# Performance work log

Hardware: AMD Instinct MI355X
Metric: run time of the kernel (lower is better)

The kernel has to match this reference:

```python
import jax, jax.numpy as jnp
import numpy as np

B, H, S, D = 2, 16, 2048, 64


def setup_inputs() -> dict:
    key = jax.random.key(0)
    kq, kk, kv = jax.random.split(key, 3)
    Q = jax.random.normal(kq, (B, H, S, D), dtype=jnp.float32)
    K = jax.random.normal(kk, (B, H, S, D), dtype=jnp.float32)
    V = jax.random.normal(kv, (B, H, S, D), dtype=jnp.float32)
    # causal mask: True = masked out (matches torch masked_fill_ semantics)
    causal = ~jnp.tril(jnp.ones((S, S), dtype=bool))
    mask = jnp.broadcast_to(causal, (B, H, S, S))
    return {"Q": Q, "K": K, "V": V, "mask": mask}


def reference(Q, K, V, mask):
    d_q = Q.shape[-1]
    scale = 1.0 / np.sqrt(d_q).astype(np.float32)
    # scores: (B, H, S, S)
    scores = jnp.einsum('bhqd,bhkd->bhqk', Q, K) * scale
    scores = jnp.where(mask, jnp.float32(-1e9), scores)
    attention = jax.nn.softmax(scores, axis=-1)
    context = jnp.einsum('bhqk,bhkd->bhqd', attention, V)
    return (context, attention)
```

## Files before the change

kernel.cpp:

```cpp
#include <hip/hip_runtime.h>
#include <hip/hip_bf16.h>


constexpr int SEQ = 2048;
constexpr int HD  = 64;
constexpr int NHEADS = 32;
constexpr int QT  = 64;
constexpr int NT  = SEQ / QT;

typedef __bf16 bf16x8 __attribute__((ext_vector_type(8)));
typedef unsigned short u16x8 __attribute__((ext_vector_type(8)));
typedef unsigned short u16x4 __attribute__((ext_vector_type(4)));
typedef float f32x4 __attribute__((ext_vector_type(4)));
typedef unsigned short us;

__device__ __forceinline__ us f2bf(float x) {
  unsigned u = __builtin_bit_cast(unsigned, x);
  return (us)((u + 0x7fffu + ((u >> 16) & 1u)) >> 16);
}
__device__ __forceinline__ float bf2f(us b) {
  return __builtin_bit_cast(float, (unsigned)b << 16);
}

#define GLOAD_LDS(gp, lp)                                                        \
  __builtin_amdgcn_global_load_lds(                                             \
      (const __attribute__((address_space(1))) void*)(gp),                      \
      (__attribute__((address_space(3))) void*)(lp), 16, 0, 0)

__device__ __forceinline__ void stage8k(const us* img, us* lds, int w, int l) {
  const char* g = (const char*)img + w * 2048 + l * 16;
  char* s = (char*)lds + w * 2048;
  GLOAD_LDS(g, s);
  GLOAD_LDS(g + 1024, s + 1024);
}

__global__ void prep_kernel(const float* __restrict__ Qg,
                            const float* __restrict__ Kg,
                            const float* __restrict__ Vg,
                            us* __restrict__ ws) {
  const int tile = blockIdx.x & (NT - 1);
  const int bh   = blockIdx.x >> 5;
  const int t = threadIdx.x;
  const size_t tOff = ((size_t)bh * SEQ + (size_t)tile * QT) * HD;
  us* Qi = ws + ((size_t)bh * NT + tile) * 4096;
  us* Ki = Qi + (size_t)NHEADS * NT * 4096;
  us* Vi = Ki + (size_t)NHEADS * NT * 4096;

  #pragma unroll
  for (int g0 = 0; g0 < 2; ++g0) {
    const int g = t + 256 * g0;
    const int r = g >> 3, c8 = g & 7;
    const int cp = (8 * c8) ^ ((r & 7) << 3);
    const float* qs = Qg + tOff + (size_t)r * HD + cp;
    const float* ks = Kg + tOff + (size_t)r * HD + cp;
    u16x8 q, k;
    #pragma unroll
    for (int j = 0; j < 8; ++j) { q[j] = f2bf(qs[j]); k[j] = f2bf(ks[j]); }
    *(u16x8*)(Qi + 8 * g) = q;
    *(u16x8*)(Ki + 8 * g) = k;
  }
  #pragma unroll
  for (int g0 = 0; g0 < 2; ++g0) {
    const int g = t + 256 * g0;
    const int d = g >> 3, k8 = g & 7;
    const int kp = (8 * k8) ^ ((d & 7) << 3);
    const float* vs = Vg + tOff + d;
    u16x8 v;
    #pragma unroll
    for (int j = 0; j < 8; ++j) v[j] = f2bf(vs[(size_t)(kp + j) * HD]);
    *(u16x8*)(Vi + 8 * g) = v;
  }
}

__launch_bounds__(256, 3)
__global__ void attn_main(const us* __restrict__ ws, float* __restrict__ out) {
  const int fb = blockIdx.x;
  const int bh = fb & (NHEADS - 1);
  const int pi = fb >> 5;
  const int t  = threadIdx.x;
  const int l  = t & 63;
  const int w  = t >> 6;
  const int l16 = l & 15;
  const int lg  = l >> 4;

  __shared__ __align__(16) us Ks[2][4096];
  __shared__ __align__(16) us Vs[2][4096];
  __shared__ __align__(16) us Ps[4][1024];

  const us* Qi = ws + (size_t)bh * NT * 4096;
  const us* Ki = Qi + (size_t)NHEADS * NT * 4096;
  const us* Vi = Ki + (size_t)NHEADS * NT * 4096;

  float* ctx = out + (size_t)bh * SEQ * HD;
  float* att = out + (size_t)NHEADS * SEQ * HD + (size_t)bh * SEQ * SEQ;

  const float KC = 0.18033688011112042f;

  for (int half = 0; half < 2; ++half) {
    const int qt = half ? (NT - 1 - pi) : pi;
    const int qbase = qt * QT;
    const int qg = qbase + w * 16 + l16;

    stage8k(Ki, Ks[0], w, l);
    bf16x8 aq[2];
    {
      const int qr = w * 16 + l16;
      #pragma unroll
      for (int ks = 0; ks < 2; ++ks) {
        const int idx = (qr * 64 + ks * 32 + lg * 8) ^ ((qr & 7) << 3);
        aq[ks] = __builtin_bit_cast(bf16x8, *(const u16x8*)(&Qi[(size_t)qt * 4096 + idx]));
      }
    }
    {
      const int zc0 = (qt + 1) * QT;
      const int nz4 = (SEQ - zc0) >> 2;
      for (int rr = 0; rr < QT; ++rr) {
        float* rowp = att + (size_t)(qbase + rr) * SEQ + zc0;
        for (int c = t; c < nz4; c += 256)
          __builtin_nontemporal_store((f32x4){0.f, 0.f, 0.f, 0.f}, (f32x4*)(rowp + 4 * c));
      }
    }
    __syncthreads();

    float rsum = 0.f;
    {
      int cur = 0;
      for (int kt = 0; kt <= qt; ++kt) {
        if (kt < qt) stage8k(Ki + (size_t)(kt + 1) * 4096, Ks[cur ^ 1], w, l);
        const us* krb = Ks[cur];
        const int kb = kt * QT;
        #pragma unroll
        for (int ct = 0; ct < 4; ++ct) {
          f32x4 acc = {0.f, 0.f, 0.f, 0.f};
          #pragma unroll
          for (int ks = 0; ks < 2; ++ks) {
            const int kr = ct * 16 + l16;
            const int idx = (kr * 64 + ks * 32 + lg * 8) ^ ((kr & 7) << 3);
            bf16x8 bk = __builtin_bit_cast(bf16x8, *(const u16x8*)(&krb[idx]));
            acc = __builtin_amdgcn_mfma_f32_16x16x32_bf16(bk, aq[ks], acc, 0, 0, 0);
          }
          const int kg0 = kb + ct * 16 + lg * 4;
          #pragma unroll
          for (int rr = 0; rr < 4; ++rr) {
            float e = __builtin_amdgcn_exp2f(acc[rr] * KC);
            rsum += (kg0 + rr <= qg) ? e : 0.f;
          }
        }
        __syncthreads();
        cur ^= 1;
      }
    }
    stage8k(Ki, Ks[0], w, l);
    stage8k(Vi, Vs[0], w, l);
    rsum += __shfl_xor(rsum, 16);
    rsum += __shfl_xor(rsum, 32);
    const float inv = 1.f / rsum;
    __syncthreads();

    f32x4 oacc[4];
    #pragma unroll
    for (int ct = 0; ct < 4; ++ct) oacc[ct] = (f32x4){0.f, 0.f, 0.f, 0.f};

    {
      int cur = 0;
      for (int kt = 0; kt <= qt; ++kt) {
        if (kt < qt) {
          stage8k(Ki + (size_t)(kt + 1) * 4096, Ks[cur ^ 1], w, l);
          stage8k(Vi + (size_t)(kt + 1) * 4096, Vs[cur ^ 1], w, l);
        }
        __builtin_amdgcn_sched_barrier(0);
        const us* krb = Ks[cur];
        const us* vrb = Vs[cur];
        const int kb = kt * QT;

        #pragma unroll
        for (int ct = 0; ct < 4; ++ct) {
          f32x4 acc = {0.f, 0.f, 0.f, 0.f};
          #pragma unroll
          for (int ks = 0; ks < 2; ++ks) {
            const int kr = ct * 16 + l16;
            const int idx = (kr * 64 + ks * 32 + lg * 8) ^ ((kr & 7) << 3);
            bf16x8 bk = __builtin_bit_cast(bf16x8, *(const u16x8*)(&krb[idx]));
            acc = __builtin_amdgcn_mfma_f32_16x16x32_bf16(bk, aq[ks], acc, 0, 0, 0);
          }
          const int kg0 = kb + ct * 16 + lg * 4;
          u16x4 pb;
          #pragma unroll
          for (int rr = 0; rr < 4; ++rr) {
            float e = __builtin_amdgcn_exp2f(acc[rr] * KC) * inv;
            pb[rr] = f2bf((kg0 + rr <= qg) ? e : 0.f);
          }
          const int pidx = (l16 * 64 + ct * 16 + lg * 4) ^ ((l16 & 7) << 3);
          *(u16x4*)(&Ps[w][pidx]) = pb;
        }

        #pragma unroll
        for (int j = 0; j < 4; ++j) {
          const int rloc = lg + 4 * j;
          const int idx = (rloc * 64 + 4 * l16) ^ ((rloc & 7) << 3);
          u16x4 p4 = *(const u16x4*)(&Ps[w][idx]);
          f32x4 pv = { bf2f(p4[0]), bf2f(p4[1]), bf2f(p4[2]), bf2f(p4[3]) };
          __builtin_nontemporal_store(pv,
              (f32x4*)(att + (size_t)(qbase + w * 16 + rloc) * SEQ + kb + 4 * l16));
        }

        bf16x8 pa[2];
        #pragma unroll
        for (int ks = 0; ks < 2; ++ks) {
          const int pidx = (l16 * 64 + ks * 32 + lg * 8) ^ ((l16 & 7) << 3);
          pa[ks] = __builtin_bit_cast(bf16x8, *(const u16x8*)(&Ps[w][pidx]));
        }
        #pragma unroll
        for (int ct = 0; ct < 4; ++ct) {
          #pragma unroll
          for (int ks = 0; ks < 2; ++ks) {
            const int dr = ct * 16 + l16;
            const int vidx = (dr * 64 + ks * 32 + lg * 8) ^ ((dr & 7) << 3);
            bf16x8 av = __builtin_bit_cast(bf16x8, *(const u16x8*)(&vrb[vidx]));
            oacc[ct] = __builtin_amdgcn_mfma_f32_16x16x32_bf16(av, pa[ks], oacc[ct], 0, 0, 0);
          }
        }

        if (kt < qt) {
          asm volatile("s_waitcnt vmcnt(4) lgkmcnt(0)" ::: "memory");
        } else {
          asm volatile("s_waitcnt lgkmcnt(0)" ::: "memory");
        }
        __builtin_amdgcn_s_barrier();
        __builtin_amdgcn_sched_barrier(0);
        cur ^= 1;
      }
    }

    #pragma unroll
    for (int ct = 0; ct < 4; ++ct)
      __builtin_nontemporal_store(oacc[ct],
          (f32x4*)(ctx + (size_t)qg * HD + ct * 16 + lg * 4));
  }
}

__launch_bounds__(256, 2)
__global__ void attn_fallback(const float* __restrict__ Qg,
                              const float* __restrict__ Kg,
                              const float* __restrict__ Vg,
                              float* __restrict__ out) {
  const int fb = blockIdx.x;
  const int bh = fb & (NHEADS - 1);
  const int pi = fb >> 5;
  const int t  = threadIdx.x;
  const int l  = t & 63;
  const int w  = t >> 6;
  const int l16 = l & 15;
  const int lg  = l >> 4;

  __shared__ __align__(16) us Qs[QT * HD];
  __shared__ __align__(16) us Ks[QT * HD];
  __shared__ __align__(16) us Vs[QT * HD];
  __shared__ __align__(16) us Ps[4][16 * QT];

  const size_t hoff = (size_t)bh * SEQ * HD;
  const float* Qh = Qg + hoff;
  const float* Kh = Kg + hoff;
  const float* Vh = Vg + hoff;
  float* ctx = out + hoff;
  float* att = out + (size_t)NHEADS * SEQ * HD + (size_t)bh * SEQ * SEQ;

  auto load_tile = [&](const float* src, f32x4 (&reg)[4]) {
    #pragma unroll
    for (int j = 0; j < 4; ++j) {
      const int f = t + 256 * j;
      reg[j] = *(const f32x4*)(src + (size_t)(f >> 4) * HD + 4 * (f & 15));
    }
  };
  auto write_k = [&](const f32x4 (&reg)[4], us* dst) {
    #pragma unroll
    for (int j = 0; j < 4; ++j) {
      const int f = t + 256 * j;
      const int rr = f >> 4, c4 = f & 15;
      const int idx = (rr * 64 + 4 * c4) ^ ((rr & 7) << 3);
      u16x4 b = { f2bf(reg[j].x), f2bf(reg[j].y), f2bf(reg[j].z), f2bf(reg[j].w) };
      *(u16x4*)(&dst[idx]) = b;
    }
  };
  auto write_vv = [&](const f32x4 (&reg)[4], us* dst) {
    #pragma unroll
    for (int j = 0; j < 4; ++j) {
      const int f = t + 256 * j;
      const int rr = f >> 4, c4 = f & 15;
      const int idx = (rr * 64 + 4 * c4) ^ (((rr >> 3) & 3) << 4);
      u16x4 b = { f2bf(reg[j].x), f2bf(reg[j].y), f2bf(reg[j].z), f2bf(reg[j].w) };
      *(u16x4*)(&dst[idx]) = b;
    }
  };

  const float sc = 0.125f;

  for (int half = 0; half < 2; ++half) {
    const int qt = half ? (NT - 1 - pi) : pi;
    const int qbase = qt * QT;
    const int qg = qbase + w * 16 + l16;

    __syncthreads();
    {
      const int zc0 = (qt + 1) * QT;
      const int nz4 = (SEQ - zc0) >> 2;
      for (int rr = 0; rr < QT; ++rr) {
        float* rowp = att + (size_t)(qbase + rr) * SEQ + zc0;
        for (int c = t; c < nz4; c += 256)
          __builtin_nontemporal_store((f32x4){0.f, 0.f, 0.f, 0.f}, (f32x4*)(rowp + 4 * c));
      }
    }
    {
      f32x4 qreg[4];
      load_tile(Qh + (size_t)qbase * HD, qreg);
      write_k(qreg, Qs);
    }
    __syncthreads();

    bf16x8 aq[2];
    #pragma unroll
    for (int ks = 0; ks < 2; ++ks) {
      const int qr = w * 16 + l16;
      const int idx = (qr * 64 + ks * 32 + lg * 8) ^ ((qr & 7) << 3);
      aq[ks] = __builtin_bit_cast(bf16x8, *(const u16x8*)(&Qs[idx]));
    }

    float rsum = 0.f;
    {
      f32x4 kreg[4];
      load_tile(Kh, kreg);
      write_k(kreg, Ks);
      __syncthreads();
      for (int kt = 0; kt <= qt; ++kt) {
        if (kt < qt) load_tile(Kh + (size_t)(kt + 1) * QT * HD, kreg);
        const int kb = kt * QT;
        #pragma unroll
        for (int ct = 0; ct < 4; ++ct) {
          f32x4 acc = {0.f, 0.f, 0.f, 0.f};
          #pragma unroll
          for (int ks = 0; ks < 2; ++ks) {
            const int kr = ct * 16 + l16;
            const int idx = (kr * 64 + ks * 32 + lg * 8) ^ ((kr & 7) << 3);
            bf16x8 bk = __builtin_bit_cast(bf16x8, *(const u16x8*)(&Ks[idx]));
            acc = __builtin_amdgcn_mfma_f32_16x16x32_bf16(bk, aq[ks], acc, 0, 0, 0);
          }
          const int kg0 = kb + ct * 16 + lg * 4;
          #pragma unroll
          for (int rr = 0; rr < 4; ++rr) {
            float e = __expf(acc[rr] * sc);
            rsum += (kg0 + rr <= qg) ? e : 0.f;
          }
        }
        __syncthreads();
        if (kt < qt) write_k(kreg, Ks);
        __syncthreads();
      }
    }
    rsum += __shfl_xor(rsum, 16);
    rsum += __shfl_xor(rsum, 32);
    const float inv = 1.f / rsum;

    f32x4 oacc[4];
    #pragma unroll
    for (int ct = 0; ct < 4; ++ct) oacc[ct] = (f32x4){0.f, 0.f, 0.f, 0.f};

    {
      f32x4 kreg[4], vreg[4];
      load_tile(Kh, kreg);
      load_tile(Vh, vreg);
      write_k(kreg, Ks);
      write_vv(vreg, Vs);
      __syncthreads();
      for (int kt = 0; kt <= qt; ++kt) {
        if (kt < qt) {
          load_tile(Kh + (size_t)(kt + 1) * QT * HD, kreg);
          load_tile(Vh + (size_t)(kt + 1) * QT * HD, vreg);
        }
        const int kb = kt * QT;
        #pragma unroll
        for (int ct = 0; ct < 4; ++ct) {
          f32x4 acc = {0.f, 0.f, 0.f, 0.f};
          #pragma unroll
          for (int ks = 0; ks < 2; ++ks) {
            const int kr = ct * 16 + l16;
            const int idx = (kr * 64 + ks * 32 + lg * 8) ^ ((kr & 7) << 3);
            bf16x8 bk = __builtin_bit_cast(bf16x8, *(const u16x8*)(&Ks[idx]));
            acc = __builtin_amdgcn_mfma_f32_16x16x32_bf16(bk, aq[ks], acc, 0, 0, 0);
          }
          const int kg0 = kb + ct * 16 + lg * 4;
          u16x4 pb;
          #pragma unroll
          for (int rr = 0; rr < 4; ++rr) {
            float e = __expf(acc[rr] * sc) * inv;
            pb[rr] = f2bf((kg0 + rr <= qg) ? e : 0.f);
          }
          const int pidx = (l16 * 64 + ct * 16 + lg * 4) ^ ((l16 & 7) << 3);
          *(u16x4*)(&Ps[w][pidx]) = pb;
        }
        #pragma unroll
        for (int ct = 0; ct < 4; ++ct) {
          #pragma unroll
          for (int ks = 0; ks < 2; ++ks) {
            const int key0 = ks * 32 + lg * 8;
            const int pidx = (l16 * 64 + key0) ^ ((l16 & 7) << 3);
            bf16x8 pa = __builtin_bit_cast(bf16x8, *(const u16x8*)(&Ps[w][pidx]));
            bf16x8 av;
            const int dcol = ct * 16 + l16;
            const int xorv = ((key0 >> 3) & 3) << 4;
            #pragma unroll
            for (int j = 0; j < 8; ++j)
              av[j] = __builtin_bit_cast(__bf16, Vs[((key0 + j) * 64 + dcol) ^ xorv]);
            oacc[ct] = __builtin_amdgcn_mfma_f32_16x16x32_bf16(av, pa, oacc[ct], 0, 0, 0);
          }
        }
        __syncthreads();
        #pragma unroll
        for (int j = 0; j < 4; ++j) {
          const int f = t + 256 * j;
          const int rr = f >> 4, c4 = f & 15;
          const int ww = rr >> 4, qr = rr & 15;
          const int idx = (qr * 64 + 4 * c4) ^ ((qr & 7) << 3);
          u16x4 pb = *(const u16x4*)(&Ps[ww][idx]);
          f32x4 pv = { bf2f(pb[0]), bf2f(pb[1]), bf2f(pb[2]), bf2f(pb[3]) };
          __builtin_nontemporal_store(pv,
              (f32x4*)(att + (size_t)(qbase + rr) * SEQ + kb + 4 * c4));
        }
        if (kt < qt) {
          write_k(kreg, Ks);
          write_vv(vreg, Vs);
        }
        __syncthreads();
      }
    }
    #pragma unroll
    for (int ct = 0; ct < 4; ++ct)
      *(f32x4*)(ctx + (size_t)qg * HD + ct * 16 + lg * 4) = oacc[ct];
  }
}

extern "C" void kernel_launch(void* const* d_in, const int* in_sizes, int n_in,
                              void* d_out, int out_size, void* d_ws, size_t ws_size,
                              hipStream_t stream) {
  const float* Q = (const float*)d_in[0];
  const float* K = (const float*)d_in[1];
  const float* V = (const float*)d_in[2];
  float* out = (float*)d_out;
  const size_t NEED = (size_t)3 * NHEADS * NT * 4096 * sizeof(us);
  if (ws_size >= NEED && d_ws != nullptr) {
    us* wsp = (us*)d_ws;
    prep_kernel<<<dim3(NHEADS * NT), dim3(256), 0, stream>>>(Q, K, V, wsp);
    attn_main<<<dim3(NT / 2 * NHEADS), dim3(256), 0, stream>>>(wsp, out);
  } else {
    attn_fallback<<<dim3(NT / 2 * NHEADS), dim3(256), 0, stream>>>(Q, K, V, out);
  }
}
```

Measured before the change: 145.4 us.

## Fuse row-sum passes for paired low/high query tiles and remap block order

Each block now handles its low and high causal query tiles together. It computes both tiles' softmax denominators in one sweep over K, so the low tile reuses the K tiles staged for the high tile instead of loading them again. Block-to-tile mapping is also permuted so that the upper half of the grid walks tiles in reverse order. The manual waitcnt/s_barrier pipelining in the P·V phase is replaced by a plain __syncthreads, which may lose overlap. Holding two sets of Q fragments and accumulators raises register pressure.

```diff
diff --git a/kernel.cpp b/kernel.cpp
--- a/kernel.cpp
+++ b/kernel.cpp
@@ -76,7 +76,9 @@
 __global__ void attn_main(const us* __restrict__ ws, float* __restrict__ out) {
   const int fb = blockIdx.x;
   const int bh = fb & (NHEADS - 1);
-  const int pi = fb >> 5;
+  const int pr = (fb >> 5) & 7;
+  const int pi = (fb >> 8) ? (15 - pr) : pr;
+  const int lo = pi, hi = NT - 1 - pi;
   const int t  = threadIdx.x;
   const int l  = t & 63;
   const int w  = t >> 6;
@@ -96,147 +98,163 @@
 
   const float KC = 0.18033688011112042f;
 
-  for (int half = 0; half < 2; ++half) {
-    const int qt = half ? (NT - 1 - pi) : pi;
-    const int qbase = qt * QT;
-    const int qg = qbase + w * 16 + l16;
-
-    stage8k(Ki, Ks[0], w, l);
-    bf16x8 aq[2];
-    {
-      const int qr = w * 16 + l16;
-      #pragma unroll
-      for (int ks = 0; ks < 2; ++ks) {
-        const int idx = (qr * 64 + ks * 32 + lg * 8) ^ ((qr & 7) << 3);
-        aq[ks] = __builtin_bit_cast(bf16x8, *(const u16x8*)(&Qi[(size_t)qt * 4096 + idx]));
-      }
-    }
-    {
+  bf16x8 aql[2], aqh[2];
+  {
+    const int qr = w * 16 + l16;
+    #pragma unroll
+    for (int ks = 0; ks < 2; ++ks) {
+      const int idx = (qr * 64 + ks * 32 + lg * 8) ^ ((qr & 7) << 3);
+      aql[ks] = __builtin_bit_cast(bf16x8, *(const u16x8*)(&Qi[(size_t)lo * 4096 + idx]));
+      aqh[ks] = __builtin_bit_cast(bf16x8, *(const u16x8*)(&Qi[(size_t)hi * 4096 + idx]));
+    }
+  }
+  const int qg_lo = lo * QT + w * 16 + l16;
+  const int qg_hi = hi * QT + w * 16 + l16;
+
+  stage8k(Ki, Ks[0], w, l);
+  {
+    auto zfill = [&](int qt) {
+      const int qb = qt * QT;
       const int zc0 = (qt + 1) * QT;
       const int nz4 = (SEQ - zc0) >> 2;
       for (int rr = 0; rr < QT; ++rr) {
-        float* rowp = att + (size_t)(qbase + rr) * SEQ + zc0;
+        float* rowp = att + (size_t)(qb + rr) * SEQ + zc0;
         for (int c = t; c < nz4; c += 256)
           __builtin_nontemporal_store((f32x4){0.f, 0.f, 0.f, 0.f}, (f32x4*)(rowp + 4 * c));
       }
-    }
-    __syncthreads();
-
-    float rsum = 0.f;
-    {
-      int cur = 0;
-      for (int kt = 0; kt <= qt; ++kt) {
-        if (kt < qt) stage8k(Ki + (size_t)(kt + 1) * 4096, Ks[cur ^ 1], w, l);
-        const us* krb = Ks[cur];
-        const int kb = kt * QT;
-        #pragma unroll
-        for (int ct = 0; ct < 4; ++ct) {
-          f32x4 acc = {0.f, 0.f, 0.f, 0.f};
-          #pragma unroll
-          for (int ks = 0; ks < 2; ++ks) {
-            const int kr = ct * 16 + l16;
-            const int idx = (kr * 64 + ks * 32 + lg * 8) ^ ((kr & 7) << 3);
-            bf16x8 bk = __builtin_bit_cast(bf16x8, *(const u16x8*)(&krb[idx]));
-            acc = __builtin_amdgcn_mfma_f32_16x16x32_bf16(bk, aq[ks], acc, 0, 0, 0);
-          }
-          const int kg0 = kb + ct * 16 + lg * 4;
-          #pragma unroll
-          for (int rr = 0; rr < 4; ++rr) {
-            float e = __builtin_amdgcn_exp2f(acc[rr] * KC);
-            rsum += (kg0 + rr <= qg) ? e : 0.f;
-          }
-        }
-        __syncthreads();
-        cur ^= 1;
-      }
-    }
-    stage8k(Ki, Ks[0], w, l);
-    stage8k(Vi, Vs[0], w, l);
-    rsum += __shfl_xor(rsum, 16);
-    rsum += __shfl_xor(rsum, 32);
-    const float inv = 1.f / rsum;
-    __syncthreads();
-
+    };
+    zfill(lo);
+    zfill(hi);
+  }
+  __syncthreads();
+
+  float rs_lo = 0.f, rs_hi = 0.f;
+  {
+    int cur = 0;
+    for (int kt = 0; kt <= hi; ++kt) {
+      if (kt < hi) stage8k(Ki + (size_t)(kt + 1) * 4096, Ks[cur ^ 1], w, l);
+      const us* krb = Ks[cur];
+      const int kb = kt * QT;
+      const bool loact = (kt <= lo);
+      #pragma unroll
+      for (int ct = 0; ct < 4; ++ct) {
+        f32x4 acch = {0.f, 0.f, 0.f, 0.f};
+        f32x4 accl = {0.f, 0.f, 0.f, 0.f};
+        #pragma unroll
+        for (int ks = 0; ks < 2; ++ks) {
+          const int kr = ct * 16 + l16;
+          const int idx = (kr * 64 + ks * 32 + lg * 8) ^ ((kr & 7) << 3);
+          bf16x8 bk = __builtin_bit_cast(bf16x8, *(const u16x8*)(&krb[idx]));
+          acch = __builtin_amdgcn_mfma_f32_16x16x32_bf16(bk, aqh[ks], acch, 0, 0, 0);
+          if (loact)
+            accl = __builtin_amdgcn_mfma_f32_16x16x32_bf16(bk, aql[ks], accl, 0, 0, 0);
+        }
+        const int kg0 = kb + ct * 16 + lg * 4;
+        #pragma unroll
+        for (int rr = 0; rr < 4; ++rr)
+          rs_hi += (kg0 + rr <= qg_hi) ? __builtin_amdgcn_exp2f(acch[rr] * KC) : 0.f;
+        if (loact) {
+          #pragma unroll
+          for (int rr = 0; rr < 4; ++rr)
+            rs_lo += (kg0 + rr <= qg_lo) ? __builtin_amdgcn_exp2f(accl[rr] * KC) : 0.f;
+        }
+      }
+      __syncthreads();
+      cur ^= 1;
+    }
+  }
+  stage8k(Ki, Ks[0], w, l);
+  stage8k(Vi, Vs[0], w, l);
+  rs_lo += __shfl_xor(rs_lo, 16);
+  rs_lo += __shfl_xor(rs_lo, 32);
+  rs_hi += __shfl_xor(rs_hi, 16);
+  rs_hi += __shfl_xor(rs_hi, 32);
+  const float inv_lo = 1.f / rs_lo;
+  const float inv_hi = 1.f / rs_hi;
+  __syncthreads();
+
+  auto phase2 = [&](int qt, const bf16x8 (&aq)[2], float inv) {
+    const int qbase = qt * QT;
+    const int qg = qbase + w * 16 + l16;
     f32x4 oacc[4];
     #pragma unroll
     for (int ct = 0; ct < 4; ++ct) oacc[ct] = (f32x4){0.f, 0.f, 0.f, 0.f};
 
-    {
-      int cur = 0;
-      for (int kt = 0; kt <= qt; ++kt) {
-        if (kt < qt) {
-          stage8k(Ki + (size_t)(kt + 1) * 4096, Ks[cur ^ 1], w, l);
-          stage8k(Vi + (size_t)(kt + 1) * 4096, Vs[cur ^ 1], w, l);
-        }
-        __builtin_amdgcn_sched_barrier(0);
-        const us* krb = Ks[cur];
-        const us* vrb = Vs[cur];
-        const int kb = kt * QT;
-
-        #pragma unroll
-        for (int ct = 0; ct < 4; ++ct) {
-          f32x4 acc = {0.f, 0.f, 0.f, 0.f};
-          #pragma unroll
-          for (int ks = 0; ks < 2; ++ks) {
-            const int kr = ct * 16 + l16;
-            const int idx = (kr * 64 + ks * 32 + lg * 8) ^ ((kr & 7) << 3);
-            bf16x8 bk = __builtin_bit_cast(bf16x8, *(const u16x8*)(&krb[idx]));
-            acc = __builtin_amdgcn_mfma_f32_16x16x32_bf16(bk, aq[ks], acc, 0, 0, 0);
-          }
-          const int kg0 = kb + ct * 16 + lg * 4;
-          u16x4 pb;
-          #pragma unroll
-          for (int rr = 0; rr < 4; ++rr) {
-            float e = __builtin_amdgcn_exp2f(acc[rr] * KC) * inv;
-            pb[rr] = f2bf((kg0 + rr <= qg) ? e : 0.f);
-          }
-          const int pidx = (l16 * 64 + ct * 16 + lg * 4) ^ ((l16 & 7) << 3);
-          *(u16x4*)(&Ps[w][pidx]) = pb;
-        }
-
-        #pragma unroll
-        for (int j = 0; j < 4; ++j) {
-          const int rloc = lg + 4 * j;
-          const int idx = (rloc * 64 + 4 * l16) ^ ((rloc & 7) << 3);
-          u16x4 p4 = *(const u16x4*)(&Ps[w][idx]);
-          f32x4 pv = { bf2f(p4[0]), bf2f(p4[1]), bf2f(p4[2]), bf2f(p4[3]) };
-          __builtin_nontemporal_store(pv,
-              (f32x4*)(att + (size_t)(qbase + w * 16 + rloc) * SEQ + kb + 4 * l16));
-        }
-
-        bf16x8 pa[2];
+    int cur = 0;
+    for (int kt = 0; kt <= qt; ++kt) {
+      if (kt < qt) {
+        stage8k(Ki + (size_t)(kt + 1) * 4096, Ks[cur ^ 1], w, l);
+        stage8k(Vi + (size_t)(kt + 1) * 4096, Vs[cur ^ 1], w, l);
+      }
+      const us* krb = Ks[cur];
+      const us* vrb = Vs[cur];
+      const int kb = kt * QT;
+
+      #pragma unroll
+      for (int ct = 0; ct < 4; ++ct) {
+        f32x4 acc = {0.f, 0.f, 0.f, 0.f};
         #pragma unroll
         for (int ks = 0; ks < 2; ++ks) {
-          const int pidx = (l16 * 64 + ks * 32 + lg * 8) ^ ((l16 & 7) << 3);
-          pa[ks] = __builtin_bit_cast(bf16x8, *(const u16x8*)(&Ps[w][pidx]));
-        }
-        #pragma unroll
-        for (int ct = 0; ct < 4; ++ct) {
-          #pragma unroll
-          for (int ks = 0; ks < 2; ++ks) {
-            const int dr = ct * 16 + l16;
-            const int vidx = (dr * 64 + ks * 32 + lg * 8) ^ ((dr & 7) << 3);
-            bf16x8 av = __builtin_bit_cast(bf16x8, *(const u16x8*)(&vrb[vidx]));
-            oacc[ct] = __builtin_amdgcn_mfma_f32_16x16x32_bf16(av, pa[ks], oacc[ct], 0, 0, 0);
-          }
-        }
-
-        if (kt < qt) {
-          asm volatile("s_waitcnt vmcnt(4) lgkmcnt(0)" ::: "memory");
-        } else {
-          asm volatile("s_waitcnt lgkmcnt(0)" ::: "memory");
-        }
-        __builtin_amdgcn_s_barrier();
-        __builtin_amdgcn_sched_barrier(0);
-        cur ^= 1;
-      }
+          const int kr = ct * 16 + l16;
+          const int idx = (kr * 64 + ks * 32 + lg * 8) ^ ((kr & 7) << 3);
+          bf16x8 bk = __builtin_bit_cast(bf16x8, *(const u16x8*)(&krb[idx]));
+          acc = __builtin_amdgcn_mfma_f32_16x16x32_bf16(bk, aq[ks], acc, 0, 0, 0);
+        }
+        const int kg0 = kb + ct * 16 + lg * 4;
+        u16x4 pb;
+        #pragma unroll
+        for (int rr = 0; rr < 4; ++rr) {
+          float e = __builtin_amdgcn_exp2f(acc[rr] * KC) * inv;
+          pb[rr] = f2bf((kg0 + rr <= qg) ? e : 0.f);
+        }
+        const int pidx = (l16 * 64 + ct * 16 + lg * 4) ^ ((l16 & 7) << 3);
+        *(u16x4*)(&Ps[w][pidx]) = pb;
+      }
+
+      #pragma unroll
+      for (int j = 0; j < 4; ++j) {
+        const int rloc = lg + 4 * j;
+        const int idx = (rloc * 64 + 4 * l16) ^ ((rloc & 7) << 3);
+        u16x4 p4 = *(const u16x4*)(&Ps[w][idx]);
+        f32x4 pv = { bf2f(p4[0]), bf2f(p4[1]), bf2f(p4[2]), bf2f(p4[3]) };
+        __builtin_nontemporal_store(pv,
+            (f32x4*)(att + (size_t)(qbase + w * 16 + rloc) * SEQ + kb + 4 * l16));
+      }
+
+      bf16x8 pa[2];
+      #pragma unroll
+      for (int ks = 0; ks < 2; ++ks) {
+        const int pidx = (l16 * 64 + ks * 32 + lg * 8) ^ ((l16 & 7) << 3);
+        pa[ks] = __builtin_bit_cast(bf16x8, *(const u16x8*)(&Ps[w][pidx]));
+      }
+      #pragma unroll
+      for (int ct = 0; ct < 4; ++ct) {
+        #pragma unroll
+        for (int ks = 0; ks < 2; ++ks) {
+          const int dr = ct * 16 + l16;
+          const int vidx = (dr * 64 + ks * 32 + lg * 8) ^ ((dr & 7) << 3);
+          bf16x8 av = __builtin_bit_cast(bf16x8, *(const u16x8*)(&vrb[vidx]));
+          oacc[ct] = __builtin_amdgcn_mfma_f32_16x16x32_bf16(av, pa[ks], oacc[ct], 0, 0, 0);
+        }
+      }
+
+      __syncthreads();
+      cur ^= 1;
     }
 
     #pragma unroll
     for (int ct = 0; ct < 4; ++ct)
       __builtin_nontemporal_store(oacc[ct],
           (f32x4*)(ctx + (size_t)qg * HD + ct * 16 + lg * 4));
-  }
+  };
+
+  phase2(lo, aql, inv_lo);
+
+  stage8k(Ki, Ks[0], w, l);
+  stage8k(Vi, Vs[0], w, l);
+  __syncthreads();
+
+  phase2(hi, aqh, inv_hi);
 }
 
 __launch_bounds__(256, 2)
```

Result: slower. 158.7 us (+9.1%).

## Interleave causal zero-fill stores with score pass and stage Q via LDS

Applied to the files above, without the earlier changes.

Moves the zeroing of the masked upper-triangle attention region for both query tiles out of a serial prologue and spreads it in chunks across the first sixteen key iterations of the second half's row-sum pass, so the stores overlap with MFMA work. Q is now staged into LDS with the async loader instead of being read directly from global memory. The PV loop drops its hand-tuned vmcnt wait in favour of a plain __syncthreads, which may reduce load/compute overlap there. The zero-fill covers 124 chunks with clamping, so the last chunk is written repeatedly.

```diff
diff --git a/kernel.cpp b/kernel.cpp
--- a/kernel.cpp
+++ b/kernel.cpp
@@ -83,6 +83,7 @@
   const int l16 = l & 15;
   const int lg  = l >> 4;
 
+  __shared__ __align__(16) us Qs[4096];
   __shared__ __align__(16) us Ks[2][4096];
   __shared__ __align__(16) us Vs[2][4096];
   __shared__ __align__(16) us Ps[4][1024];
@@ -96,37 +97,43 @@
 
   const float KC = 0.18033688011112042f;
 
+  const int lo = pi, hi = NT - 1 - pi;
+  const int n_lo = (31 - lo) * 16;
+  auto zchunk = [&](int cc) {
+    const int id = cc * 256 + t;
+    const int vr = id / 496;
+    const int off = id - vr * 496;
+    size_t eoff;
+    if (off < n_lo)
+      eoff = (size_t)(lo * QT + vr) * SEQ + (lo + 1) * QT + 4 * off;
+    else
+      eoff = (size_t)(hi * QT + vr) * SEQ + (hi + 1) * QT + 4 * (off - n_lo);
+    __builtin_nontemporal_store((f32x4){0.f, 0.f, 0.f, 0.f}, (f32x4*)(att + eoff));
+  };
+
   for (int half = 0; half < 2; ++half) {
-    const int qt = half ? (NT - 1 - pi) : pi;
+    const int qt = half ? hi : lo;
     const int qbase = qt * QT;
     const int qg = qbase + w * 16 + l16;
 
+    stage8k(Qi + (size_t)qt * 4096, Qs, w, l);
     stage8k(Ki, Ks[0], w, l);
+    __syncthreads();
+
     bf16x8 aq[2];
-    {
+    #pragma unroll
+    for (int ks = 0; ks < 2; ++ks) {
       const int qr = w * 16 + l16;
-      #pragma unroll
-      for (int ks = 0; ks < 2; ++ks) {
-        const int idx = (qr * 64 + ks * 32 + lg * 8) ^ ((qr & 7) << 3);
-        aq[ks] = __builtin_bit_cast(bf16x8, *(const u16x8*)(&Qi[(size_t)qt * 4096 + idx]));
-      }
-    }
-    {
-      const int zc0 = (qt + 1) * QT;
-      const int nz4 = (SEQ - zc0) >> 2;
-      for (int rr = 0; rr < QT; ++rr) {
-        float* rowp = att + (size_t)(qbase + rr) * SEQ + zc0;
-        for (int c = t; c < nz4; c += 256)
-          __builtin_nontemporal_store((f32x4){0.f, 0.f, 0.f, 0.f}, (f32x4*)(rowp + 4 * c));
-      }
-    }
-    __syncthreads();
+      const int idx = (qr * 64 + ks * 32 + lg * 8) ^ ((qr & 7) << 3);
+      aq[ks] = __builtin_bit_cast(bf16x8, *(const u16x8*)(&Qs[idx]));
+    }
 
     float rsum = 0.f;
     {
       int cur = 0;
       for (int kt = 0; kt <= qt; ++kt) {
         if (kt < qt) stage8k(Ki + (size_t)(kt + 1) * 4096, Ks[cur ^ 1], w, l);
+        __builtin_amdgcn_sched_barrier(0);
         const us* krb = Ks[cur];
         const int kb = kt * QT;
         #pragma unroll
@@ -146,7 +153,18 @@
             rsum += (kg0 + rr <= qg) ? e : 0.f;
           }
         }
-        __syncthreads();
+        if (half == 1 && kt < 16) {
+          #pragma unroll
+          for (int c = 0; c < 8; ++c) {
+            int cc = kt * 8 + c;
+            zchunk(cc < 124 ? cc : 123);
+          }
+          asm volatile("s_waitcnt vmcnt(8) lgkmcnt(0)" ::: "memory");
+          __builtin_amdgcn_s_barrier();
+          __builtin_amdgcn_sched_barrier(0);
+        } else {
+          __syncthreads();
+        }
         cur ^= 1;
       }
     }
@@ -168,7 +186,6 @@
           stage8k(Ki + (size_t)(kt + 1) * 4096, Ks[cur ^ 1], w, l);
           stage8k(Vi + (size_t)(kt + 1) * 4096, Vs[cur ^ 1], w, l);
         }
-        __builtin_amdgcn_sched_barrier(0);
         const us* krb = Ks[cur];
         const us* vrb = Vs[cur];
         const int kb = kt * QT;
@@ -221,13 +238,7 @@
           }
         }
 
-        if (kt < qt) {
-          asm volatile("s_waitcnt vmcnt(4) lgkmcnt(0)" ::: "memory");
-        } else {
-          asm volatile("s_waitcnt lgkmcnt(0)" ::: "memory");
-        }
-        __builtin_amdgcn_s_barrier();
-        __builtin_amdgcn_sched_barrier(0);
+        __syncthreads();
         cur ^= 1;
       }
     }
```

After: 165.0 us. 1.13x slower.

## Deepen K/V LDS pipeline to four stages and defer attention stores

Applied to the files above, without the earlier changes.

Replaces double-buffered K/V staging with a 4-slot ring that prefetches three tiles ahead, using explicit vmcnt waits before barriers instead of full syncthreads. Q is now staged through LDS instead of loaded directly from global memory. Each attention-tile store is deferred by one iteration so global writes overlap the next tile's compute. LDS use roughly doubles, so occupancy is lowered to 2 blocks per CU, and the hand-computed vmcnt counts have to match the number of outstanding loads and stores exactly.

```diff
diff --git a/kernel.cpp b/kernel.cpp
--- a/kernel.cpp
+++ b/kernel.cpp
@@ -21,6 +21,7 @@
 __device__ __forceinline__ float bf2f(us b) {
   return __builtin_bit_cast(float, (unsigned)b << 16);
 }
+__device__ __forceinline__ int imin(int a, int b) { return a < b ? a : b; }
 
 #define GLOAD_LDS(gp, lp)                                                        \
   __builtin_amdgcn_global_load_lds(                                             \
@@ -32,6 +33,19 @@
   char* s = (char*)lds + w * 2048;
   GLOAD_LDS(g, s);
   GLOAD_LDS(g + 1024, s + 1024);
+}
+
+__device__ __forceinline__ void wait_n_barrier(int n) {
+  switch (n) {
+    case 0:  asm volatile("s_waitcnt vmcnt(0) lgkmcnt(0)"  ::: "memory"); break;
+    case 2:  asm volatile("s_waitcnt vmcnt(2) lgkmcnt(0)"  ::: "memory"); break;
+    case 4:  asm volatile("s_waitcnt vmcnt(4) lgkmcnt(0)"  ::: "memory"); break;
+    case 8:  asm volatile("s_waitcnt vmcnt(8) lgkmcnt(0)"  ::: "memory"); break;
+    case 12: asm volatile("s_waitcnt vmcnt(12) lgkmcnt(0)" ::: "memory"); break;
+    default: asm volatile("s_waitcnt vmcnt(16) lgkmcnt(0)" ::: "memory"); break;
+  }
+  __builtin_amdgcn_s_barrier();
+  __builtin_amdgcn_sched_barrier(0);
 }
 
 __global__ void prep_kernel(const float* __restrict__ Qg,
@@ -72,7 +86,7 @@
   }
 }
 
-__launch_bounds__(256, 3)
+__launch_bounds__(256, 2)
 __global__ void attn_main(const us* __restrict__ ws, float* __restrict__ out) {
   const int fb = blockIdx.x;
   const int bh = fb & (NHEADS - 1);
@@ -83,8 +97,9 @@
   const int l16 = l & 15;
   const int lg  = l >> 4;
 
-  __shared__ __align__(16) us Ks[2][4096];
-  __shared__ __align__(16) us Vs[2][4096];
+  __shared__ __align__(16) us Qs[4096];
+  __shared__ __align__(16) us Ks[4][4096];
+  __shared__ __align__(16) us Vs[4][4096];
   __shared__ __align__(16) us Ps[4][1024];
 
   const us* Qi = ws + (size_t)bh * NT * 4096;
@@ -101,16 +116,6 @@
     const int qbase = qt * QT;
     const int qg = qbase + w * 16 + l16;
 
-    stage8k(Ki, Ks[0], w, l);
-    bf16x8 aq[2];
-    {
-      const int qr = w * 16 + l16;
-      #pragma unroll
-      for (int ks = 0; ks < 2; ++ks) {
-        const int idx = (qr * 64 + ks * 32 + lg * 8) ^ ((qr & 7) << 3);
-        aq[ks] = __builtin_bit_cast(bf16x8, *(const u16x8*)(&Qi[(size_t)qt * 4096 + idx]));
-      }
-    }
     {
       const int zc0 = (qt + 1) * QT;
       const int nz4 = (SEQ - zc0) >> 2;
@@ -120,118 +125,128 @@
           __builtin_nontemporal_store((f32x4){0.f, 0.f, 0.f, 0.f}, (f32x4*)(rowp + 4 * c));
       }
     }
-    __syncthreads();
+    stage8k(Qi + (size_t)qt * 4096, Qs, w, l);
+    stage8k(Ki, Ks[0], w, l);
+    if (qt >= 1) stage8k(Ki + 4096, Ks[1], w, l);
+    if (qt >= 2) stage8k(Ki + 2 * 4096, Ks[2], w, l);
+    wait_n_barrier(0);
+
+    bf16x8 aq[2];
+    #pragma unroll
+    for (int ks = 0; ks < 2; ++ks) {
+      const int qr = w * 16 + l16;
+      const int idx = (qr * 64 + ks * 32 + lg * 8) ^ ((qr & 7) << 3);
+      aq[ks] = __builtin_bit_cast(bf16x8, *(const u16x8*)(&Qs[idx]));
+    }
 
     float rsum = 0.f;
-    {
-      int cur = 0;
-      for (int kt = 0; kt <= qt; ++kt) {
-        if (kt < qt) stage8k(Ki + (size_t)(kt + 1) * 4096, Ks[cur ^ 1], w, l);
-        const us* krb = Ks[cur];
-        const int kb = kt * QT;
-        #pragma unroll
-        for (int ct = 0; ct < 4; ++ct) {
-          f32x4 acc = {0.f, 0.f, 0.f, 0.f};
-          #pragma unroll
-          for (int ks = 0; ks < 2; ++ks) {
-            const int kr = ct * 16 + l16;
-            const int idx = (kr * 64 + ks * 32 + lg * 8) ^ ((kr & 7) << 3);
-            bf16x8 bk = __builtin_bit_cast(bf16x8, *(const u16x8*)(&krb[idx]));
-            acc = __builtin_amdgcn_mfma_f32_16x16x32_bf16(bk, aq[ks], acc, 0, 0, 0);
-          }
-          const int kg0 = kb + ct * 16 + lg * 4;
-          #pragma unroll
-          for (int rr = 0; rr < 4; ++rr) {
-            float e = __builtin_amdgcn_exp2f(acc[rr] * KC);
-            rsum += (kg0 + rr <= qg) ? e : 0.f;
-          }
-        }
-        __syncthreads();
-        cur ^= 1;
-      }
-    }
+    for (int kt = 0; kt <= qt; ++kt) {
+      if (kt + 3 <= qt) stage8k(Ki + (size_t)(kt + 3) * 4096, Ks[(kt + 3) & 3], w, l);
+      __builtin_amdgcn_sched_barrier(0);
+      const us* krb = Ks[kt & 3];
+      const int kb = kt * QT;
+      #pragma unroll
+      for (int ct = 0; ct < 4; ++ct) {
+        f32x4 acc = {0.f, 0.f, 0.f, 0.f};
+        #pragma unroll
+        for (int ks = 0; ks < 2; ++ks) {
+          const int kr = ct * 16 + l16;
+          const int idx = (kr * 64 + ks * 32 + lg * 8) ^ ((kr & 7) << 3);
+          bf16x8 bk = __builtin_bit_cast(bf16x8, *(const u16x8*)(&krb[idx]));
+          acc = __builtin_amdgcn_mfma_f32_16x16x32_bf16(bk, aq[ks], acc, 0, 0, 0);
+        }
+        const int kg0 = kb + ct * 16 + lg * 4;
+        #pragma unroll
+        for (int rr = 0; rr < 4; ++rr) {
+          float e = __builtin_amdgcn_exp2f(acc[rr] * KC);
+          rsum += (kg0 + rr <= qg) ? e : 0.f;
+        }
+      }
+      const int n1 = (kt == qt) ? 0 : 2 * imin(imin(kt + 3, qt) - kt - 1, 2);
+      wait_n_barrier(n1);
+    }
+
     stage8k(Ki, Ks[0], w, l);
     stage8k(Vi, Vs[0], w, l);
+    if (qt >= 1) { stage8k(Ki + 4096, Ks[1], w, l); stage8k(Vi + 4096, Vs[1], w, l); }
+    if (qt >= 2) { stage8k(Ki + 2 * 4096, Ks[2], w, l); stage8k(Vi + 2 * 4096, Vs[2], w, l); }
     rsum += __shfl_xor(rsum, 16);
     rsum += __shfl_xor(rsum, 32);
     const float inv = 1.f / rsum;
-    __syncthreads();
+    wait_n_barrier(4 * imin(2, qt));
 
     f32x4 oacc[4];
     #pragma unroll
     for (int ct = 0; ct < 4; ++ct) oacc[ct] = (f32x4){0.f, 0.f, 0.f, 0.f};
 
-    {
-      int cur = 0;
-      for (int kt = 0; kt <= qt; ++kt) {
-        if (kt < qt) {
-          stage8k(Ki + (size_t)(kt + 1) * 4096, Ks[cur ^ 1], w, l);
-          stage8k(Vi + (size_t)(kt + 1) * 4096, Vs[cur ^ 1], w, l);
-        }
-        __builtin_amdgcn_sched_barrier(0);
-        const us* krb = Ks[cur];
-        const us* vrb = Vs[cur];
-        const int kb = kt * QT;
-
-        #pragma unroll
-        for (int ct = 0; ct < 4; ++ct) {
-          f32x4 acc = {0.f, 0.f, 0.f, 0.f};
-          #pragma unroll
-          for (int ks = 0; ks < 2; ++ks) {
-            const int kr = ct * 16 + l16;
-            const int idx = (kr * 64 + ks * 32 + lg * 8) ^ ((kr & 7) << 3);
-            bf16x8 bk = __builtin_bit_cast(bf16x8, *(const u16x8*)(&krb[idx]));
-            acc = __builtin_amdgcn_mfma_f32_16x16x32_bf16(bk, aq[ks], acc, 0, 0, 0);
-          }
-          const int kg0 = kb + ct * 16 + lg * 4;
-          u16x4 pb;
-          #pragma unroll
-          for (int rr = 0; rr < 4; ++rr) {
-            float e = __builtin_amdgcn_exp2f(acc[rr] * KC) * inv;
-            pb[rr] = f2bf((kg0 + rr <= qg) ? e : 0.f);
-          }
-          const int pidx = (l16 * 64 + ct * 16 + lg * 4) ^ ((l16 & 7) << 3);
-          *(u16x4*)(&Ps[w][pidx]) = pb;
-        }
-
-        #pragma unroll
-        for (int j = 0; j < 4; ++j) {
-          const int rloc = lg + 4 * j;
-          const int idx = (rloc * 64 + 4 * l16) ^ ((rloc & 7) << 3);
-          u16x4 p4 = *(const u16x4*)(&Ps[w][idx]);
-          f32x4 pv = { bf2f(p4[0]), bf2f(p4[1]), bf2f(p4[2]), bf2f(p4[3]) };
-          __builtin_nontemporal_store(pv,
-              (f32x4*)(att + (size_t)(qbase + w * 16 + rloc) * SEQ + kb + 4 * l16));
-        }
-
-        bf16x8 pa[2];
+    auto att_store = [&](int src_kt) {
+      #pragma unroll
+      for (int j = 0; j < 4; ++j) {
+        const int rloc = lg + 4 * j;
+        const int idx = (rloc * 64 + 4 * l16) ^ ((rloc & 7) << 3);
+        u16x4 p4 = *(const u16x4*)(&Ps[w][idx]);
+        f32x4 pv = { bf2f(p4[0]), bf2f(p4[1]), bf2f(p4[2]), bf2f(p4[3]) };
+        __builtin_nontemporal_store(pv,
+            (f32x4*)(att + (size_t)(qbase + w * 16 + rloc) * SEQ + src_kt * QT + 4 * l16));
+      }
+    };
+
+    for (int kt = 0; kt <= qt; ++kt) {
+      if (kt > 0) att_store(kt - 1);
+      __builtin_amdgcn_sched_barrier(0);
+      if (kt + 3 <= qt) {
+        stage8k(Ki + (size_t)(kt + 3) * 4096, Ks[(kt + 3) & 3], w, l);
+        stage8k(Vi + (size_t)(kt + 3) * 4096, Vs[(kt + 3) & 3], w, l);
+      }
+      __builtin_amdgcn_sched_barrier(0);
+      const us* krb = Ks[kt & 3];
+      const us* vrb = Vs[kt & 3];
+      const int kb = kt * QT;
+
+      #pragma unroll
+      for (int ct = 0; ct < 4; ++ct) {
+        f32x4 acc = {0.f, 0.f, 0.f, 0.f};
         #pragma unroll
         for (int ks = 0; ks < 2; ++ks) {
-          const int pidx = (l16 * 64 + ks * 32 + lg * 8) ^ ((l16 & 7) << 3);
-          pa[ks] = __builtin_bit_cast(bf16x8, *(const u16x8*)(&Ps[w][pidx]));
-        }
-        #pragma unroll
-        for (int ct = 0; ct < 4; ++ct) {
-          #pragma unroll
-          for (int ks = 0; ks < 2; ++ks) {
-            const int dr = ct * 16 + l16;
-            const int vidx = (dr * 64 + ks * 32 + lg * 8) ^ ((dr & 7) << 3);
-            bf16x8 av = __builtin_bit_cast(bf16x8, *(const u16x8*)(&vrb[vidx]));
-            oacc[ct] = __builtin_amdgcn_mfma_f32_16x16x32_bf16(av, pa[ks], oacc[ct], 0, 0, 0);
-          }
-        }
-
-        if (kt < qt) {
-          asm volatile("s_waitcnt vmcnt(4) lgkmcnt(0)" ::: "memory");
-        } else {
-          asm volatile("s_waitcnt lgkmcnt(0)" ::: "memory");
-        }
-        __builtin_amdgcn_s_barrier();
-        __builtin_amdgcn_sched_barrier(0);
-        cur ^= 1;
-      }
-    }
-
+          const int kr = ct * 16 + l16;
+          const int idx = (kr * 64 + ks * 32 + lg * 8) ^ ((kr & 7) << 3);
+          bf16x8 bk = __builtin_bit_cast(bf16x8, *(const u16x8*)(&krb[idx]));
+          acc = __builtin_amdgcn_mfma_f32_16x16x32_bf16(bk, aq[ks], acc, 0, 0, 0);
+        }
+        const int kg0 = kb + ct * 16 + lg * 4;
+        u16x4 pb;
+        #pragma unroll
+        for (int rr = 0; rr < 4; ++rr) {
+          float e = __builtin_amdgcn_exp2f(acc[rr] * KC) * inv;
+          pb[rr] = f2bf((kg0 + rr <= qg) ? e : 0.f);
+        }
+        const int pidx = (l16 * 64 + ct * 16 + lg * 4) ^ ((l16 & 7) << 3);
+        *(u16x4*)(&Ps[w][pidx]) = pb;
+      }
+
+      bf16x8 pa[2];
+      #pragma unroll
+      for (int ks = 0; ks < 2; ++ks) {
+        const int pidx = (l16 * 64 + ks * 32 + lg * 8) ^ ((l16 & 7) << 3);
+        pa[ks] = __builtin_bit_cast(bf16x8, *(const u16x8*)(&Ps[w][pidx]));
+      }
+      #pragma unroll
+      for (int ct = 0; ct < 4; ++ct) {
+        #pragma unroll
+        for (int ks = 0; ks < 2; ++ks) {
+          const int dr = ct * 16 + l16;
+          const int vidx = (dr * 64 + ks * 32 + lg * 8) ^ ((dr & 7) << 3);
+          bf16x8 av = __builtin_bit_cast(bf16x8, *(const u16x8*)(&vrb[vidx]));
+          oacc[ct] = __builtin_amdgcn_mfma_f32_16x16x32_bf16(av, pa[ks], oacc[ct], 0, 0, 0);
+        }
+      }
+
+      const int n2 = (kt == qt) ? 0
+                   : 4 * (imin(imin(kt + 3, qt) - kt - 1, 2) + imin(kt, 2));
+      wait_n_barrier(n2);
+    }
+
+    att_store(qt);
     #pragma unroll
     for (int ct = 0; ct < 4; ++ct)
       __builtin_nontemporal_store(oacc[ct],
```

After: 147.1 us. Within noise of the previous version (+1.2%).
